# Performance work log

Hardware: AMD Instinct MI355X
Metric: run time of the kernel (lower is better)

## Reference

```python
import jax, jax.numpy as jnp
import numpy as np

B, T, D, DE, S, P = 16384, 2, 1024, 512, 4, 4  # batch, tasks, inp_dim, expt_dim, share, specific


def setup_inputs() -> dict:
    key = jax.random.key(0)
    ks = jax.random.split(key, 8)
    sc = 0.02
    return {
        "x0": jax.random.normal(ks[0], (B, D), jnp.float32),
        "x1": jax.random.normal(ks[1], (B, D), jnp.float32),
        "W_share": jax.random.normal(ks[2], (S, D, DE), jnp.float32) * sc,
        "b_share": jnp.zeros((S, DE), jnp.float32),
        "W_spcf": jax.random.normal(ks[3], (T, P, D, DE), jnp.float32) * sc,
        "b_spcf": jnp.zeros((T, P, DE), jnp.float32),
        "W_gate": jax.random.normal(ks[4], (T, D, S + P), jnp.float32) * sc,
        "b_gate": jnp.zeros((T, S + P), jnp.float32),
    }


def reference(x0, x1, W_share, b_share, W_spcf, b_spcf, W_gate, b_gate):
    # cat_x: [B, T, D]
    x = jnp.stack([x0, x1], axis=1)
    # per-task gate over all S+P experts: [B, T, S+P]
    gates = jax.nn.softmax(jnp.einsum("btd,tde->bte", x, W_gate) + b_gate, axis=-1)
    # shared experts applied to every task's input: [B, T, S, DE]
    share = jax.nn.relu(jnp.einsum("btd,sdf->btsf", x, W_share) + b_share[None, None])
    # task-specific experts applied to their own task input: [B, T, P, DE]
    spcf = jax.nn.relu(jnp.einsum("btd,tpdf->btpf", x, W_spcf) + b_spcf[None])
    experts = jnp.concatenate([share, spcf], axis=2)  # [B, T, S+P, DE]
    # softmax-gated mixture: [B, T, DE] (== list of per-task [B, DE] in the original)
    return jnp.einsum("bte,btef->btf", gates, experts)
```

## Files before the change

kernel.cpp:

```cpp
#include <hip/hip_runtime.h>
#include <stdint.h>

#define kB  16384
#define kD  1024
#define kDE 512

typedef __bf16 bf16x8 __attribute__((ext_vector_type(8)));
typedef float  f32x4  __attribute__((ext_vector_type(4)));

__device__ __forceinline__ unsigned short f2bf(float f) {
    union { float f; unsigned u; } v; v.f = f;
    unsigned r = v.u + 0x7FFFu + ((v.u >> 16) & 1u);
    return (unsigned short)(r >> 16);
}

__device__ __forceinline__ void async16(unsigned short* lds, const unsigned short* g) {
    __builtin_amdgcn_global_load_lds(
        (const __attribute__((address_space(1))) unsigned int*)g,
        (__attribute__((address_space(3))) unsigned int*)lds, 16, 0, 0);
}

__global__ __launch_bounds__(256) void prep_w(const float* __restrict__ Wsh,
                                              const float* __restrict__ Wsp,
                                              unsigned short* __restrict__ Wt) {
    __shared__ float tile[64][65];
    const int slot = blockIdx.z;
    const int k0 = blockIdx.x * 64;
    const int n0 = blockIdx.y * 64;
    const float* src = (slot < 4) ? (Wsh + (size_t)slot * kD * kDE)
                                  : (Wsp + (size_t)(slot - 4) * kD * kDE);
    const int tid = threadIdx.x;
    const int lr = tid >> 4, lc = (tid & 15) * 4;
#pragma unroll
    for (int i = 0; i < 4; i++) {
        const float4 v = *(const float4*)&src[(size_t)(k0 + lr + i * 16) * kDE + n0 + lc];
        tile[lr + i * 16][lc + 0] = v.x;
        tile[lr + i * 16][lc + 1] = v.y;
        tile[lr + i * 16][lc + 2] = v.z;
        tile[lr + i * 16][lc + 3] = v.w;
    }
    __syncthreads();
    const int wn = tid >> 2, wk = (tid & 3) * 16;
    unsigned short* dst = Wt + (size_t)slot * kDE * kD + (size_t)(n0 + wn) * kD + k0 + wk;
#pragma unroll
    for (int j = 0; j < 4; j++) {
        ushort4 h;
        h.x = f2bf(tile[wk + j * 4 + 0][wn]);
        h.y = f2bf(tile[wk + j * 4 + 1][wn]);
        h.z = f2bf(tile[wk + j * 4 + 2][wn]);
        h.w = f2bf(tile[wk + j * 4 + 3][wn]);
        *(ushort4*)(dst + j * 4) = h;
    }
}

__global__ __launch_bounds__(256) void conv_gate(
    const float* __restrict__ x0, const float* __restrict__ x1,
    const float* __restrict__ Wg, const float* __restrict__ bg,
    unsigned short* __restrict__ xb, float* __restrict__ g) {
    const int wid = threadIdx.x >> 6, lane = threadIdx.x & 63;
    const int r = blockIdx.x * 4 + wid;
    const int t = r >> 14, b = r & 16383;
    const float* xrow = (t ? x1 : x0) + (size_t)b * kD;
    unsigned short* xbrow = xb + (size_t)(t * kB + b) * kD;
    const float* Wgt = Wg + t * kD * 8;
    float p[8] = {0.f,0.f,0.f,0.f,0.f,0.f,0.f,0.f};
#pragma unroll
    for (int it = 0; it < 4; it++) {
        const int d0 = it * 256 + lane * 4;
        const float4 v = *(const float4*)(xrow + d0);
        ushort4 h;
        h.x = f2bf(v.x); h.y = f2bf(v.y); h.z = f2bf(v.z); h.w = f2bf(v.w);
        *(ushort4*)(xbrow + d0) = h;
        const float xv[4] = {v.x, v.y, v.z, v.w};
#pragma unroll
        for (int j = 0; j < 4; j++) {
            const float* wrow = Wgt + (size_t)(d0 + j) * 8;
            const float4 wa = *(const float4*)wrow;
            const float4 wb = *(const float4*)(wrow + 4);
            p[0] += xv[j] * wa.x; p[1] += xv[j] * wa.y;
            p[2] += xv[j] * wa.z; p[3] += xv[j] * wa.w;
            p[4] += xv[j] * wb.x; p[5] += xv[j] * wb.y;
            p[6] += xv[j] * wb.z; p[7] += xv[j] * wb.w;
        }
    }
#pragma unroll
    for (int e = 0; e < 8; e++) {
        float v = p[e];
#pragma unroll
        for (int s = 1; s < 64; s <<= 1) v += __shfl_xor(v, s, 64);
        p[e] = v;
    }
    float lg[8];
#pragma unroll
    for (int e = 0; e < 8; e++) lg[e] = p[e] + bg[t * 8 + e];
    float mx = lg[0];
#pragma unroll
    for (int e = 1; e < 8; e++) mx = fmaxf(mx, lg[e]);
    float s = 0.f;
#pragma unroll
    for (int e = 0; e < 8; e++) { lg[e] = __expf(lg[e] - mx); s += lg[e]; }
    const float inv = 1.f / s;
    if (lane == 0) {
        float* gp = g + (size_t)(t * kB + b) * 8;
        float4 g0 = {lg[0]*inv, lg[1]*inv, lg[2]*inv, lg[3]*inv};
        float4 g1 = {lg[4]*inv, lg[5]*inv, lg[6]*inv, lg[7]*inv};
        *(float4*)gp = g0;
        *(float4*)(gp + 4) = g1;
    }
}

__global__ __launch_bounds__(512, 2) void moe_gemm(
    const unsigned short* __restrict__ xb, const unsigned short* __restrict__ Wt,
    const float* __restrict__ g, const float* __restrict__ bsh,
    const float* __restrict__ bsp, float* __restrict__ out) {
    __shared__ __align__(16) unsigned short As[2][128 * 64];
    __shared__ __align__(16) unsigned short Bs[2][8 * 64 * 64];

    const int bid = blockIdx.x;
    const int swz = (bid & 7) * 256 + (bid >> 3);
    const int ct = swz & 7;
    const int rt = (swz >> 3) & 127;
    const int t  = swz >> 10;
    const int n0 = ct * 64;

    const int tid = threadIdx.x, wid = tid >> 6, lane = tid & 63;
    const int wr = wid >> 2, wc = wid & 3;

    const int swzChunk = ((lane & 7) ^ ((lane >> 3) & 7)) * 8;
    const unsigned short* aSrc = xb + (size_t)t * kB * kD +
        (size_t)(rt * 128 + wid * 16 + (lane >> 3)) * kD + swzChunk;
    const int slot = (wid < 4) ? wid : (4 + t * 4 + (wid - 4));
    const unsigned short* bSrc = Wt + (size_t)slot * kDE * kD +
        (size_t)(n0 + (lane >> 3)) * kD + swzChunk;

    const int rAbase = (wr * 64 + (lane & 15)) * 64;
    const int bOff   = (wc * 16 + (lane & 15)) * 64;
    const int lx     = lane & 7;
    const int kg     = lane >> 4;

    f32x4 acc[8][4];
#pragma unroll
    for (int e = 0; e < 8; e++)
#pragma unroll
        for (int m = 0; m < 4; m++) acc[e][m] = (f32x4){0.f, 0.f, 0.f, 0.f};

#define STAGE(buf, kt)                                                        \
    {                                                                         \
        const int k0_ = (kt) * 64;                                            \
        _Pragma("unroll")                                                     \
        for (int i = 0; i < 2; i++)                                           \
            async16(&As[buf][wid * 1024 + i * 512], aSrc + k0_ + i * 8 * kD); \
        _Pragma("unroll")                                                     \
        for (int j = 0; j < 8; j++)                                           \
            async16(&Bs[buf][wid * 4096 + j * 512], bSrc + k0_ + j * 8 * kD); \
    }

#define COMPUTE(buf)                                                          \
    {                                                                         \
        _Pragma("unroll")                                                     \
        for (int ks = 0; ks < 2; ks++) {                                      \
            const int p8 = ((ks * 4 + kg) ^ lx) * 8;                          \
            bf16x8 af[4];                                                     \
            _Pragma("unroll")                                                 \
            for (int m = 0; m < 4; m++)                                       \
                af[m] = *(const bf16x8*)&As[buf][rAbase + m * 1024 + p8];     \
            _Pragma("unroll")                                                 \
            for (int e = 0; e < 8; e++) {                                     \
                bf16x8 bf = *(const bf16x8*)&Bs[buf][e * 4096 + bOff + p8];   \
                _Pragma("unroll")                                             \
                for (int m = 0; m < 4; m++)                                   \
                    acc[e][m] = __builtin_amdgcn_mfma_f32_16x16x32_bf16(      \
                        af[m], bf, acc[e][m], 0, 0, 0);                       \
            }                                                                 \
        }                                                                     \
    }

    STAGE(0, 0);
    for (int kt2 = 0; kt2 < 8; ++kt2) {
        STAGE(1, kt2 * 2 + 1);
        asm volatile("s_waitcnt vmcnt(10)" ::: "memory");
        __builtin_amdgcn_s_barrier();
        COMPUTE(0);
        __builtin_amdgcn_s_barrier();
        STAGE(0, (kt2 * 2 + 2) & 15);
        asm volatile("s_waitcnt vmcnt(10)" ::: "memory");
        __builtin_amdgcn_s_barrier();
        COMPUTE(1);
        __builtin_amdgcn_s_barrier();
    }
    asm volatile("s_waitcnt vmcnt(0)" ::: "memory");

#undef STAGE
#undef COMPUTE

    const int col = n0 + wc * 16 + (lane & 15);
    float bv[8];
#pragma unroll
    for (int e = 0; e < 8; e++)
        bv[e] = (e < 4) ? bsh[e * kDE + col] : bsp[(t * 4 + (e - 4)) * kDE + col];

#pragma unroll
    for (int m = 0; m < 4; m++) {
        const int r0 = rt * 128 + wr * 64 + m * 16 + kg * 4;
#pragma unroll
        for (int q = 0; q < 4; q++) {
            const float* gp = g + ((size_t)t * kB + r0 + q) * 8;
            const float4 ga = *(const float4*)gp;
            const float4 gb = *(const float4*)(gp + 4);
            float s = ga.x * fmaxf(acc[0][m][q] + bv[0], 0.f)
                    + ga.y * fmaxf(acc[1][m][q] + bv[1], 0.f)
                    + ga.z * fmaxf(acc[2][m][q] + bv[2], 0.f)
                    + ga.w * fmaxf(acc[3][m][q] + bv[3], 0.f)
                    + gb.x * fmaxf(acc[4][m][q] + bv[4], 0.f)
                    + gb.y * fmaxf(acc[5][m][q] + bv[5], 0.f)
                    + gb.z * fmaxf(acc[6][m][q] + bv[6], 0.f)
                    + gb.w * fmaxf(acc[7][m][q] + bv[7], 0.f);
            out[((size_t)(r0 + q) * 2 + t) * kDE + col] = s;
        }
    }
}

extern "C" void kernel_launch(void* const* d_in, const int* in_sizes, int n_in,
                              void* d_out, int out_size, void* d_ws, size_t ws_size,
                              hipStream_t stream) {
    const float* x0  = (const float*)d_in[0];
    const float* x1  = (const float*)d_in[1];
    const float* Wsh = (const float*)d_in[2];
    const float* bsh = (const float*)d_in[3];
    const float* Wsp = (const float*)d_in[4];
    const float* bsp = (const float*)d_in[5];
    const float* Wg  = (const float*)d_in[6];
    const float* bg  = (const float*)d_in[7];
    float* out = (float*)d_out;

    char* ws = (char*)d_ws;
    unsigned short* xb = (unsigned short*)ws;
    unsigned short* Wt = (unsigned short*)(ws + 67108864);
    float* g  = (float*)(ws + 67108864 + 12582912);

    prep_w<<<dim3(16, 8, 12), dim3(256), 0, stream>>>(Wsh, Wsp, Wt);
    conv_gate<<<dim3(8192), dim3(256), 0, stream>>>(x0, x1, Wg, bg, xb, g);
    moe_gemm<<<dim3(2048), dim3(512), 0, stream>>>(xb, Wt, g, bsh, bsp, out);
}
```

Baseline: 410.7 us.

## Split GEMM workgroup into producer and consumer waves for warp specialization

The MoE GEMM workgroup grows from 8 to 10 waves. Eight consumer waves only run MFMA compute from LDS, and two producer waves issue all global-to-LDS async loads for the next stage. This is meant to decouple memory issue from compute so loads overlap MFMA work without consumer waves stalling on vmcnt. In exchange, launch bounds drop to one workgroup per CU. Each producer wave now issues four times as many loads and waits fully each stage, which may reduce overlap and occupancy.

```diff
diff --git a/kernel.cpp b/kernel.cpp
--- a/kernel.cpp
+++ b/kernel.cpp
@@ -109,7 +109,7 @@
     }
 }
 
-__global__ __launch_bounds__(512, 2) void moe_gemm(
+__global__ __launch_bounds__(640, 1) void moe_gemm(
     const unsigned short* __restrict__ xb, const unsigned short* __restrict__ Wt,
     const float* __restrict__ g, const float* __restrict__ bsh,
     const float* __restrict__ bsp, float* __restrict__ out) {
@@ -124,14 +124,23 @@
     const int n0 = ct * 64;
 
     const int tid = threadIdx.x, wid = tid >> 6, lane = tid & 63;
-    const int wr = wid >> 2, wc = wid & 3;
+    const bool consumer = (wid < 8);
+    const int wr = (wid >> 2) & 1, wc = wid & 3;
 
     const int swzChunk = ((lane & 7) ^ ((lane >> 3) & 7)) * 8;
-    const unsigned short* aSrc = xb + (size_t)t * kB * kD +
-        (size_t)(rt * 128 + wid * 16 + (lane >> 3)) * kD + swzChunk;
-    const int slot = (wid < 4) ? wid : (4 + t * 4 + (wid - 4));
-    const unsigned short* bSrc = Wt + (size_t)slot * kDE * kD +
-        (size_t)(n0 + (lane >> 3)) * kD + swzChunk;
+
+    const int p4 = consumer ? 0 : (wid - 8) * 4;
+    const unsigned short* aP[4];
+    const unsigned short* bP[4];
+#pragma unroll
+    for (int jj = 0; jj < 4; jj++) {
+        const int w = p4 + jj;
+        aP[jj] = xb + (size_t)t * kB * kD +
+                 (size_t)(rt * 128 + w * 16 + (lane >> 3)) * kD + swzChunk;
+        const int slotW = (w < 4) ? w : (4 + t * 4 + (w - 4));
+        bP[jj] = Wt + (size_t)slotW * kDE * kD +
+                 (size_t)(n0 + (lane >> 3)) * kD + swzChunk;
+    }
 
     const int rAbase = (wr * 64 + (lane & 15)) * 64;
     const int bOff   = (wc * 16 + (lane & 15)) * 64;
@@ -144,18 +153,22 @@
 #pragma unroll
         for (int m = 0; m < 4; m++) acc[e][m] = (f32x4){0.f, 0.f, 0.f, 0.f};
 
-#define STAGE(buf, kt)                                                        \
+#define P_STAGE(buf, ktn)                                                     \
     {                                                                         \
-        const int k0_ = (kt) * 64;                                            \
         _Pragma("unroll")                                                     \
-        for (int i = 0; i < 2; i++)                                           \
-            async16(&As[buf][wid * 1024 + i * 512], aSrc + k0_ + i * 8 * kD); \
-        _Pragma("unroll")                                                     \
-        for (int j = 0; j < 8; j++)                                           \
-            async16(&Bs[buf][wid * 4096 + j * 512], bSrc + k0_ + j * 8 * kD); \
-    }
-
-#define COMPUTE(buf)                                                          \
+        for (int jj = 0; jj < 4; jj++) {                                      \
+            async16(&As[buf][(p4 + jj) * 1024], aP[jj] + (ktn) * 64);         \
+            async16(&As[buf][(p4 + jj) * 1024 + 512],                         \
+                    aP[jj] + (ktn) * 64 + 8 * kD);                            \
+            _Pragma("unroll")                                                 \
+            for (int j = 0; j < 8; j++)                                       \
+                async16(&Bs[buf][(p4 + jj) * 4096 + j * 512],                 \
+                        bP[jj] + (ktn) * 64 + j * 8 * kD);                    \
+        }                                                                     \
+        asm volatile("s_waitcnt vmcnt(0)" ::: "memory");                      \
+    }
+
+#define C_COMPUTE(buf)                                                        \
     {                                                                         \
         _Pragma("unroll")                                                     \
         for (int ks = 0; ks < 2; ks++) {                                      \
@@ -175,23 +188,25 @@
         }                                                                     \
     }
 
-    STAGE(0, 0);
+    if (!consumer) P_STAGE(0, 0);
+
     for (int kt2 = 0; kt2 < 8; ++kt2) {
-        STAGE(1, kt2 * 2 + 1);
-        asm volatile("s_waitcnt vmcnt(10)" ::: "memory");
         __builtin_amdgcn_s_barrier();
-        COMPUTE(0);
+        __builtin_amdgcn_sched_barrier(0);
+        if (consumer) { C_COMPUTE(0); }
+        else          { P_STAGE(1, kt2 * 2 + 1); }
+        __builtin_amdgcn_sched_barrier(0);
         __builtin_amdgcn_s_barrier();
-        STAGE(0, (kt2 * 2 + 2) & 15);
-        asm volatile("s_waitcnt vmcnt(10)" ::: "memory");
-        __builtin_amdgcn_s_barrier();
-        COMPUTE(1);
-        __builtin_amdgcn_s_barrier();
-    }
-    asm volatile("s_waitcnt vmcnt(0)" ::: "memory");
-
-#undef STAGE
-#undef COMPUTE
+        __builtin_amdgcn_sched_barrier(0);
+        if (consumer) { C_COMPUTE(1); }
+        else          { P_STAGE(0, (kt2 * 2 + 2) & 15); }
+        __builtin_amdgcn_sched_barrier(0);
+    }
+
+#undef P_STAGE
+#undef C_COMPUTE
+
+    if (!consumer) return;
 
     const int col = n0 + wc * 16 + (lane & 15);
     float bv[8];
@@ -240,5 +255,5 @@
 
     prep_w<<<dim3(16, 8, 12), dim3(256), 0, stream>>>(Wsh, Wsp, Wt);
     conv_gate<<<dim3(8192), dim3(256), 0, stream>>>(x0, x1, Wg, bg, xb, g);
-    moe_gemm<<<dim3(2048), dim3(512), 0, stream>>>(xb, Wt, g, bsh, bsp, out);
-}
+    moe_gemm<<<dim3(2048), dim3(640), 0, stream>>>(xb, Wt, g, bsh, bsp, out);
+}
```

Measured after the change: 562.2 us. 36.9% more time.
